# Kernel tuning notes

Hardware: AMD Instinct MI355X
Metric: run time of the kernel (lower is better)

## Reference

```python
import jax, jax.numpy as jnp
import numpy as np

D = 128        # sub_dim
H = D // 2     # attention hidden = max(1, sub_dim // 2)
B = 8192       # molecules per batch
N_ALL = 65536  # unique substructure embeddings
M = 409600     # total selected (mol, substructure) pairs ~ 50 per molecule
T = 12         # num_tasks


def setup_inputs() -> dict:
    key = jax.random.key(0)
    ks = jax.random.split(key, 12)
    s = 0.05
    substructure_feat = jax.random.normal(ks[0], (N_ALL, D), dtype=jnp.float32)
    feat_idx = jax.random.randint(ks[1], (M,), 0, N_ALL)
    batch_idx = jnp.sort(jax.random.randint(ks[2], (M,), 0, B))
    # attention net: Linear(D,H) -> tanh -> Linear(H,1)
    W1 = jax.random.normal(ks[3], (D, H), dtype=jnp.float32) * s
    b1 = jnp.zeros((H,), dtype=jnp.float32)
    W2 = jax.random.normal(ks[4], (H, 1), dtype=jnp.float32) * s
    b2 = jnp.zeros((1,), dtype=jnp.float32)
    # predictor: Linear(D,D) -> (dropout: identity at eval) -> relu -> Linear(D,T)
    W3 = jax.random.normal(ks[5], (D, D), dtype=jnp.float32) * s
    b3 = jnp.zeros((D,), dtype=jnp.float32)
    W4 = jax.random.normal(ks[6], (D, T), dtype=jnp.float32) * s
    b4 = jnp.zeros((T,), dtype=jnp.float32)
    return {
        "substructure_feat": substructure_feat,
        "feat_idx": feat_idx,
        "batch_idx": batch_idx,
        "dim_size": B,
        "W1": W1, "b1": b1, "W2": W2, "b2": b2,
        "W3": W3, "b3": b3, "W4": W4, "b4": b4,
    }


def reference(substructure_feat, feat_idx, batch_idx, dim_size,
              W1, b1, W2, b2, W3, b3, W4, b4):
    # gather selected substructure rows: [M, D]
    x = substructure_feat[feat_idx]
    # attention scores via tiny MLP: [M, 1]
    scores = jnp.tanh(x @ W1 + b1) @ W2 + b2
    # pyg_softmax: per-segment (per-molecule) numerically-stable softmax
    seg_max = jax.ops.segment_max(scores, batch_idx, num_segments=dim_size)  # [B,1]
    e = jnp.exp(scores - seg_max[batch_idx])
    denom = jax.ops.segment_sum(e, batch_idx, num_segments=dim_size)         # [B,1]
    alpha = e / (denom[batch_idx] + 1e-16)                                   # [M,1]
    # scatter-add pooling: [B, D]
    pooled = jax.ops.segment_sum(x * alpha, batch_idx, num_segments=dim_size)
    # predictor (dropout is identity at inference)
    h = jax.nn.relu(pooled @ W3 + b3)
    logits = h @ W4 + b4  # [B, T]
    return logits
```

## Files before the change

kernel.cpp:

```cpp
#include <hip/hip_runtime.h>
#include <hip/hip_bf16.h>
#include <math.h>

#define DD 128
#define HH 64
#define TT 12

typedef __bf16 bf16x8 __attribute__((ext_vector_type(8)));
typedef float  f32x4  __attribute__((ext_vector_type(4)));

__device__ __forceinline__ float fast_tanh(float x) {
    float ex = __expf(2.f * x);
    return (ex - 1.f) * __builtin_amdgcn_rcpf(ex + 1.f);
}

__global__ __launch_bounds__(256) void kMain(
    const int* __restrict__ bidx, int* __restrict__ segs,
    const float* __restrict__ W1, const float* __restrict__ W3,
    __bf16* __restrict__ W3f, const float* __restrict__ W4,
    __bf16* __restrict__ W4f, const float* __restrict__ feat,
    const float* __restrict__ b1, const float* __restrict__ W2,
    const float* __restrict__ b2, float* __restrict__ uexp,
    __bf16* __restrict__ ytab, int M, int B, int N, int nSetup)
{
    __shared__ __bf16 sW1f[16 * 512];
    int tid = threadIdx.x;
    if ((int)blockIdx.x < nSetup) {
        int m = blockIdx.x * 256 + tid;
        if (m < DD * DD) {
            int d = m >> 7, j = m & 127;
            int f = (d >> 5) * 8 + (j >> 4);
            int l = (((d >> 3) & 3) << 4) | (j & 15);
            W3f[f * 512 + l * 8 + (d & 7)] = (__bf16)W3[m];
        }
        if (blockIdx.x == 0) {
            for (int p = tid; p < 4 * 512; p += 256) {
                int f = p >> 9, l = (p >> 3) & 63, e = p & 7;
                int d = 32 * f + 8 * (l >> 4) + e;
                int c = l & 15;
                W4f[p] = (c < TT) ? (__bf16)W4[d * TT + c] : (__bf16)0.f;
            }
            if (tid >= 64 && tid < 128)
                reinterpret_cast<unsigned*>(ytab + (size_t)N * DD)[tid - 64] = 0u;
            if (tid == 0) uexp[N] = 0.f;
        }
        if (m < M) {
            int cur = bidx[m];
            int prev = (m == 0) ? -1 : bidx[m - 1];
            for (int b = prev + 1; b <= cur; ++b) segs[b] = m;
            if (m == M - 1)
                for (int b = cur + 1; b <= B; ++b) segs[b] = M;
        }
        return;
    }
    for (int p = tid; p < HH * DD; p += 256) {
        int d = p >> 6, j = p & 63;
        int f = (d >> 5) * 4 + (j >> 4);
        int l = (((d >> 3) & 3) << 4) | (j & 15);
        sW1f[f * 512 + l * 8 + (d & 7)] = (__bf16)W1[p];
    }
    __syncthreads();
    int sb = blockIdx.x - nSetup;
    int wave = tid >> 6, l = tid & 63;
    int m0 = (sb * 4 + wave) * 16;
    if (m0 >= N) return;
    int r = l & 15, grp = l >> 4;
    int row = min(m0 + r, N - 1);
    const float* xr = feat + (size_t)row * DD + grp * 8;

    bf16x8 a[4];
#pragma unroll
    for (int kk = 0; kk < 4; ++kk) {
        float4 u = *reinterpret_cast<const float4*>(xr + kk * 32);
        float4 v = *reinterpret_cast<const float4*>(xr + kk * 32 + 4);
        bf16x8 t;
        t[0] = (__bf16)u.x; t[1] = (__bf16)u.y; t[2] = (__bf16)u.z; t[3] = (__bf16)u.w;
        t[4] = (__bf16)v.x; t[5] = (__bf16)v.y; t[6] = (__bf16)v.z; t[7] = (__bf16)v.w;
        a[kk] = t;
    }

    f32x4 acc[4] = {};
#pragma unroll
    for (int kk = 0; kk < 4; ++kk) {
#pragma unroll
        for (int g = 0; g < 4; ++g) {
            bf16x8 bfr = *reinterpret_cast<const bf16x8*>(sW1f + (kk * 4 + g) * 512 + l * 8);
            acc[g] = __builtin_amdgcn_mfma_f32_16x16x32_bf16(a[kk], bfr, acc[g], 0, 0, 0);
        }
    }

    float part[4] = {0.f, 0.f, 0.f, 0.f};
#pragma unroll
    for (int g = 0; g < 4; ++g) {
        int j = 16 * g + r;
        float b1j = b1[j], w2j = W2[j];
#pragma unroll
        for (int q = 0; q < 4; ++q)
            part[q] = fmaf(fast_tanh(acc[g][q] + b1j), w2j, part[q]);
    }
#pragma unroll
    for (int q = 0; q < 4; ++q) {
#pragma unroll
        for (int off = 1; off < 16; off <<= 1)
            part[q] += __shfl_xor(part[q], off, 64);
    }
    float v01 = (r & 1) ? part[1] : part[0];
    float v23 = (r & 1) ? part[3] : part[2];
    float vsel = (r & 2) ? v23 : v01;
    float sc = __shfl(vsel, ((r >> 2) << 4) | r, 64);
    float ue = __expf(sc + b2[0]);
    if (grp == 0) uexp[m0 + r] = ue;
    __bf16* dst = ytab + (size_t)row * DD + grp * 8;
#pragma unroll
    for (int kk = 0; kk < 4; ++kk) {
        bf16x8 t;
#pragma unroll
        for (int e = 0; e < 8; ++e) t[e] = (__bf16)(ue * (float)a[kk][e]);
        *reinterpret_cast<bf16x8*>(dst + kk * 32) = t;
    }
}

__global__ __launch_bounds__(512) void kPoolPred(
    const __bf16* __restrict__ ytab, const int* __restrict__ fidx,
    const float* __restrict__ uexp, const int* __restrict__ segs,
    const __bf16* __restrict__ W3f, const __bf16* __restrict__ W4f,
    const float* __restrict__ b3, const float* __restrict__ b4,
    float* __restrict__ out, int B, int NZ, int M)
{
    __shared__ __bf16 psh[16][DD];
    __shared__ __bf16 hsh[16][DD];
    int tid = threadIdx.x;
    int w = tid >> 6, lane = tid & 63;
    int tile = blockIdx.x;
    int sub = lane >> 4, c16 = lane & 15;
    const __bf16* yb = ytab + c16 * 8;

#pragma unroll
    for (int s = 0; s < 2; ++s) {
        int seg = tile * 16 + 2 * w + s;
        int rowit = 2 * w + s;
        float acc[8] = {0.f, 0.f, 0.f, 0.f, 0.f, 0.f, 0.f, 0.f};
        float denl = 0.f;
        if (seg < B) {
            int start = segs[seg], end = segs[seg + 1];
            for (int base = start; base < end; base += 64) {
                int idxs[16];
#pragma unroll
                for (int i = 0; i < 16; ++i) {
                    int p = base + 4 * i + sub;
                    int v = fidx[min(p, M - 1)];
                    idxs[i] = (p < end) ? v : NZ;
                }
                int t = base + lane;
                int fi = (t < end) ? fidx[t] : NZ;
                denl += uexp[fi];
#pragma unroll
                for (int i = 0; i < 16; ++i) {
                    uint4 u4 = *reinterpret_cast<const uint4*>(yb + (size_t)idxs[i] * DD);
                    acc[0] += __builtin_bit_cast(float, u4.x << 16);
                    acc[1] += __builtin_bit_cast(float, u4.x & 0xffff0000u);
                    acc[2] += __builtin_bit_cast(float, u4.y << 16);
                    acc[3] += __builtin_bit_cast(float, u4.y & 0xffff0000u);
                    acc[4] += __builtin_bit_cast(float, u4.z << 16);
                    acc[5] += __builtin_bit_cast(float, u4.z & 0xffff0000u);
                    acc[6] += __builtin_bit_cast(float, u4.w << 16);
                    acc[7] += __builtin_bit_cast(float, u4.w & 0xffff0000u);
                }
            }
        }
        float den = denl;
#pragma unroll
        for (int off = 1; off < 64; off <<= 1) den += __shfl_xor(den, off, 64);
#pragma unroll
        for (int j = 0; j < 8; ++j) {
            acc[j] += __shfl_xor(acc[j], 16, 64);
            acc[j] += __shfl_xor(acc[j], 32, 64);
        }
        if (sub == 0) {
            float inv = 1.f / (den + 1e-16f);
            bf16x8 o;
#pragma unroll
            for (int j = 0; j < 8; ++j) o[j] = (__bf16)(acc[j] * inv);
            *reinterpret_cast<bf16x8*>(&psh[rowit][c16 * 8]) = o;
        }
    }
    __syncthreads();

    if (w != 0) return;
    int r = lane & 15, grp = lane >> 4;
    bf16x8 a[4];
#pragma unroll
    for (int kk = 0; kk < 4; ++kk)
        a[kk] = *reinterpret_cast<const bf16x8*>(&psh[r][kk * 32 + grp * 8]);

    f32x4 acc[8] = {};
#pragma unroll
    for (int kk = 0; kk < 4; ++kk) {
#pragma unroll
        for (int g = 0; g < 8; ++g) {
            bf16x8 bfr = *reinterpret_cast<const bf16x8*>(W3f + (kk * 8 + g) * 512 + lane * 8);
            acc[g] = __builtin_amdgcn_mfma_f32_16x16x32_bf16(a[kk], bfr, acc[g], 0, 0, 0);
        }
    }
#pragma unroll
    for (int g = 0; g < 8; ++g) {
        int j = 16 * g + r;
        float b3j = b3[j];
#pragma unroll
        for (int q = 0; q < 4; ++q)
            hsh[4 * grp + q][j] = (__bf16)fmaxf(acc[g][q] + b3j, 0.f);
    }
    f32x4 acc2 = {};
#pragma unroll
    for (int kk = 0; kk < 4; ++kk) {
        bf16x8 ah = *reinterpret_cast<const bf16x8*>(&hsh[r][kk * 32 + grp * 8]);
        bf16x8 bw = *reinterpret_cast<const bf16x8*>(W4f + kk * 512 + lane * 8);
        acc2 = __builtin_amdgcn_mfma_f32_16x16x32_bf16(ah, bw, acc2, 0, 0, 0);
    }
    int t = r;
    if (t < TT) {
        float b4t = b4[t];
#pragma unroll
        for (int q = 0; q < 4; ++q) {
            int ro = tile * 16 + 4 * grp + q;
            if (ro < B) out[(size_t)ro * TT + t] = acc2[q] + b4t;
        }
    }
}

extern "C" void kernel_launch(void* const* d_in, const int* in_sizes, int n_in,
                              void* d_out, int out_size, void* d_ws, size_t ws_size,
                              hipStream_t stream) {
    const float* feat = (const float*)d_in[0];
    const int*   fidx = (const int*)d_in[1];
    const int*   bidx = (const int*)d_in[2];
    const float* W1 = (const float*)d_in[4];
    const float* b1 = (const float*)d_in[5];
    const float* W2 = (const float*)d_in[6];
    const float* b2 = (const float*)d_in[7];
    const float* W3 = (const float*)d_in[8];
    const float* b3 = (const float*)d_in[9];
    const float* W4 = (const float*)d_in[10];
    const float* b4 = (const float*)d_in[11];

    int N = in_sizes[0] / DD;
    int M = in_sizes[1];
    int B = out_size / TT;
    float* out = (float*)d_out;

    char* ws = (char*)d_ws;
    size_t o = 0;
    auto alloc = [&](size_t bytes) -> char* {
        char* p = ws + o;
        o = (o + bytes + 255) & ~(size_t)255;
        return p;
    };
    float*  uexp = (float*)alloc((size_t)(N + 1) * 4);
    __bf16* W3f  = (__bf16*)alloc(32 * 512 * 2);
    __bf16* W4f  = (__bf16*)alloc(4 * 512 * 2);
    int*    segs = (int*)alloc((size_t)(B + 1) * 4);
    __bf16* ytab = (__bf16*)alloc((size_t)(N + 1) * DD * 2);

    int nSetup = (M + 255) / 256;
    int nScore = (N + 63) / 64;
    kMain<<<nSetup + nScore, 256, 0, stream>>>(bidx, segs, W1, W3, W3f, W4, W4f,
                                               feat, b1, W2, b2, uexp, ytab,
                                               M, B, N, nSetup);
    int ntiles = (B + 15) / 16;
    kPoolPred<<<ntiles, 512, 0, stream>>>(ytab, fidx, uexp, segs, W3f, W4f,
                                          b3, b4, out, B, N, M);
}
```

Before: 39.67 us.

## Process 32 rows per wave in scoring, one segment per wave in pooling

```diff
diff --git a/kernel.cpp b/kernel.cpp
--- a/kernel.cpp
+++ b/kernel.cpp
@@ -21,19 +21,20 @@
     __bf16* __restrict__ W4f, const float* __restrict__ feat,
     const float* __restrict__ b1, const float* __restrict__ W2,
     const float* __restrict__ b2, float* __restrict__ uexp,
-    __bf16* __restrict__ ytab, int M, int B, int N, int nSetup)
+    __bf16* __restrict__ ytab, int M, int B, int N, int nScore)
 {
     __shared__ __bf16 sW1f[16 * 512];
     int tid = threadIdx.x;
-    if ((int)blockIdx.x < nSetup) {
-        int m = blockIdx.x * 256 + tid;
+    if ((int)blockIdx.x >= nScore) {
+        int sb = blockIdx.x - nScore;
+        int m = sb * 256 + tid;
         if (m < DD * DD) {
             int d = m >> 7, j = m & 127;
             int f = (d >> 5) * 8 + (j >> 4);
             int l = (((d >> 3) & 3) << 4) | (j & 15);
             W3f[f * 512 + l * 8 + (d & 7)] = (__bf16)W3[m];
         }
-        if (blockIdx.x == 0) {
+        if (sb == 0) {
             for (int p = tid; p < 4 * 512; p += 256) {
                 int f = p >> 9, l = (p >> 3) & 63, e = p & 7;
                 int d = 32 * f + 8 * (l >> 4) + e;
@@ -60,67 +61,76 @@
         sW1f[f * 512 + l * 8 + (d & 7)] = (__bf16)W1[p];
     }
     __syncthreads();
-    int sb = blockIdx.x - nSetup;
     int wave = tid >> 6, l = tid & 63;
-    int m0 = (sb * 4 + wave) * 16;
+    int m0 = (blockIdx.x * 4 + wave) * 32;
     if (m0 >= N) return;
     int r = l & 15, grp = l >> 4;
-    int row = min(m0 + r, N - 1);
-    const float* xr = feat + (size_t)row * DD + grp * 8;
-
-    bf16x8 a[4];
-#pragma unroll
-    for (int kk = 0; kk < 4; ++kk) {
-        float4 u = *reinterpret_cast<const float4*>(xr + kk * 32);
-        float4 v = *reinterpret_cast<const float4*>(xr + kk * 32 + 4);
-        bf16x8 t;
-        t[0] = (__bf16)u.x; t[1] = (__bf16)u.y; t[2] = (__bf16)u.z; t[3] = (__bf16)u.w;
-        t[4] = (__bf16)v.x; t[5] = (__bf16)v.y; t[6] = (__bf16)v.z; t[7] = (__bf16)v.w;
-        a[kk] = t;
-    }
-
-    f32x4 acc[4] = {};
+
+    bf16x8 a[2][4];
+#pragma unroll
+    for (int hf = 0; hf < 2; ++hf) {
+        int row = min(m0 + hf * 16 + r, N - 1);
+        const float* xr = feat + (size_t)row * DD + grp * 8;
+#pragma unroll
+        for (int kk = 0; kk < 4; ++kk) {
+            float4 u = *reinterpret_cast<const float4*>(xr + kk * 32);
+            float4 v = *reinterpret_cast<const float4*>(xr + kk * 32 + 4);
+            bf16x8 t;
+            t[0] = (__bf16)u.x; t[1] = (__bf16)u.y; t[2] = (__bf16)u.z; t[3] = (__bf16)u.w;
+            t[4] = (__bf16)v.x; t[5] = (__bf16)v.y; t[6] = (__bf16)v.z; t[7] = (__bf16)v.w;
+            a[hf][kk] = t;
+        }
+    }
+
+    f32x4 acc[2][4] = {};
 #pragma unroll
     for (int kk = 0; kk < 4; ++kk) {
 #pragma unroll
         for (int g = 0; g < 4; ++g) {
             bf16x8 bfr = *reinterpret_cast<const bf16x8*>(sW1f + (kk * 4 + g) * 512 + l * 8);
-            acc[g] = __builtin_amdgcn_mfma_f32_16x16x32_bf16(a[kk], bfr, acc[g], 0, 0, 0);
-        }
-    }
-
-    float part[4] = {0.f, 0.f, 0.f, 0.f};
-#pragma unroll
-    for (int g = 0; g < 4; ++g) {
-        int j = 16 * g + r;
-        float b1j = b1[j], w2j = W2[j];
-#pragma unroll
-        for (int q = 0; q < 4; ++q)
-            part[q] = fmaf(fast_tanh(acc[g][q] + b1j), w2j, part[q]);
-    }
-#pragma unroll
-    for (int q = 0; q < 4; ++q) {
-#pragma unroll
-        for (int off = 1; off < 16; off <<= 1)
-            part[q] += __shfl_xor(part[q], off, 64);
-    }
-    float v01 = (r & 1) ? part[1] : part[0];
-    float v23 = (r & 1) ? part[3] : part[2];
-    float vsel = (r & 2) ? v23 : v01;
-    float sc = __shfl(vsel, ((r >> 2) << 4) | r, 64);
-    float ue = __expf(sc + b2[0]);
-    if (grp == 0) uexp[m0 + r] = ue;
-    __bf16* dst = ytab + (size_t)row * DD + grp * 8;
-#pragma unroll
-    for (int kk = 0; kk < 4; ++kk) {
-        bf16x8 t;
-#pragma unroll
-        for (int e = 0; e < 8; ++e) t[e] = (__bf16)(ue * (float)a[kk][e]);
-        *reinterpret_cast<bf16x8*>(dst + kk * 32) = t;
-    }
-}
-
-__global__ __launch_bounds__(512) void kPoolPred(
+            acc[0][g] = __builtin_amdgcn_mfma_f32_16x16x32_bf16(a[0][kk], bfr, acc[0][g], 0, 0, 0);
+            acc[1][g] = __builtin_amdgcn_mfma_f32_16x16x32_bf16(a[1][kk], bfr, acc[1][g], 0, 0, 0);
+        }
+    }
+
+    float b2v = b2[0];
+#pragma unroll
+    for (int hf = 0; hf < 2; ++hf) {
+        float part[4] = {0.f, 0.f, 0.f, 0.f};
+#pragma unroll
+        for (int g = 0; g < 4; ++g) {
+            int j = 16 * g + r;
+            float b1j = b1[j], w2j = W2[j];
+#pragma unroll
+            for (int q = 0; q < 4; ++q)
+                part[q] = fmaf(fast_tanh(acc[hf][g][q] + b1j), w2j, part[q]);
+        }
+#pragma unroll
+        for (int q = 0; q < 4; ++q) {
+#pragma unroll
+            for (int off = 1; off < 16; off <<= 1)
+                part[q] += __shfl_xor(part[q], off, 64);
+        }
+        float v01 = (r & 1) ? part[1] : part[0];
+        float v23 = (r & 1) ? part[3] : part[2];
+        float vsel = (r & 2) ? v23 : v01;
+        float sc = __shfl(vsel, ((r >> 2) << 4) | r, 64);
+        float ue = __expf(sc + b2v);
+        int mh = m0 + hf * 16;
+        if (grp == 0) uexp[mh + r] = ue;
+        int row = min(mh + r, N - 1);
+        __bf16* dst = ytab + (size_t)row * DD + grp * 8;
+#pragma unroll
+        for (int kk = 0; kk < 4; ++kk) {
+            bf16x8 t;
+#pragma unroll
+            for (int e = 0; e < 8; ++e) t[e] = (__bf16)(ue * (float)a[hf][kk][e]);
+            *reinterpret_cast<bf16x8*>(dst + kk * 32) = t;
+        }
+    }
+}
+
+__global__ __launch_bounds__(512, 6) void kPoolPred(
     const __bf16* __restrict__ ytab, const int* __restrict__ fidx,
     const float* __restrict__ uexp, const int* __restrict__ segs,
     const __bf16* __restrict__ W3f, const __bf16* __restrict__ W4f,
@@ -135,54 +145,55 @@
     int sub = lane >> 4, c16 = lane & 15;
     const __bf16* yb = ytab + c16 * 8;
 
-#pragma unroll
-    for (int s = 0; s < 2; ++s) {
-        int seg = tile * 16 + 2 * w + s;
-        int rowit = 2 * w + s;
-        float acc[8] = {0.f, 0.f, 0.f, 0.f, 0.f, 0.f, 0.f, 0.f};
-        float denl = 0.f;
-        if (seg < B) {
-            int start = segs[seg], end = segs[seg + 1];
-            for (int base = start; base < end; base += 64) {
-                int idxs[16];
-#pragma unroll
-                for (int i = 0; i < 16; ++i) {
-                    int p = base + 4 * i + sub;
-                    int v = fidx[min(p, M - 1)];
-                    idxs[i] = (p < end) ? v : NZ;
-                }
-                int t = base + lane;
-                int fi = (t < end) ? fidx[t] : NZ;
-                denl += uexp[fi];
-#pragma unroll
-                for (int i = 0; i < 16; ++i) {
-                    uint4 u4 = *reinterpret_cast<const uint4*>(yb + (size_t)idxs[i] * DD);
-                    acc[0] += __builtin_bit_cast(float, u4.x << 16);
-                    acc[1] += __builtin_bit_cast(float, u4.x & 0xffff0000u);
-                    acc[2] += __builtin_bit_cast(float, u4.y << 16);
-                    acc[3] += __builtin_bit_cast(float, u4.y & 0xffff0000u);
-                    acc[4] += __builtin_bit_cast(float, u4.z << 16);
-                    acc[5] += __builtin_bit_cast(float, u4.z & 0xffff0000u);
-                    acc[6] += __builtin_bit_cast(float, u4.w << 16);
-                    acc[7] += __builtin_bit_cast(float, u4.w & 0xffff0000u);
-                }
+    if (tid < 128) {
+        uint4 z = make_uint4(0u, 0u, 0u, 0u);
+        *reinterpret_cast<uint4*>(&psh[8 + (tid >> 4)][(tid & 15) * 8]) = z;
+    }
+
+    int seg = tile * 8 + w;
+    float acc[8] = {0.f, 0.f, 0.f, 0.f, 0.f, 0.f, 0.f, 0.f};
+    float denl = 0.f;
+    if (seg < B) {
+        int start = segs[seg], end = segs[seg + 1];
+        for (int base = start; base < end; base += 64) {
+            int idxs[16];
+#pragma unroll
+            for (int i = 0; i < 16; ++i) {
+                int p = base + 4 * i + sub;
+                int v = fidx[min(p, M - 1)];
+                idxs[i] = (p < end) ? v : NZ;
             }
-        }
-        float den = denl;
-#pragma unroll
-        for (int off = 1; off < 64; off <<= 1) den += __shfl_xor(den, off, 64);
-#pragma unroll
-        for (int j = 0; j < 8; ++j) {
-            acc[j] += __shfl_xor(acc[j], 16, 64);
-            acc[j] += __shfl_xor(acc[j], 32, 64);
-        }
-        if (sub == 0) {
-            float inv = 1.f / (den + 1e-16f);
-            bf16x8 o;
-#pragma unroll
-            for (int j = 0; j < 8; ++j) o[j] = (__bf16)(acc[j] * inv);
-            *reinterpret_cast<bf16x8*>(&psh[rowit][c16 * 8]) = o;
-        }
+            int t = base + lane;
+            int fi = (t < end) ? fidx[t] : NZ;
+            denl += uexp[fi];
+#pragma unroll
+            for (int i = 0; i < 16; ++i) {
+                uint4 u4 = *reinterpret_cast<const uint4*>(yb + (size_t)idxs[i] * DD);
+                acc[0] += __builtin_bit_cast(float, u4.x << 16);
+                acc[1] += __builtin_bit_cast(float, u4.x & 0xffff0000u);
+                acc[2] += __builtin_bit_cast(float, u4.y << 16);
+                acc[3] += __builtin_bit_cast(float, u4.y & 0xffff0000u);
+                acc[4] += __builtin_bit_cast(float, u4.z << 16);
+                acc[5] += __builtin_bit_cast(float, u4.z & 0xffff0000u);
+                acc[6] += __builtin_bit_cast(float, u4.w << 16);
+                acc[7] += __builtin_bit_cast(float, u4.w & 0xffff0000u);
+            }
+        }
+    }
+    float den = denl;
+#pragma unroll
+    for (int off = 1; off < 64; off <<= 1) den += __shfl_xor(den, off, 64);
+#pragma unroll
+    for (int j = 0; j < 8; ++j) {
+        acc[j] += __shfl_xor(acc[j], 16, 64);
+        acc[j] += __shfl_xor(acc[j], 32, 64);
+    }
+    if (sub == 0) {
+        float inv = 1.f / (den + 1e-16f);
+        bf16x8 o;
+#pragma unroll
+        for (int j = 0; j < 8; ++j) o[j] = (__bf16)(acc[j] * inv);
+        *reinterpret_cast<bf16x8*>(&psh[w][c16 * 8]) = o;
     }
     __syncthreads();
 
@@ -193,13 +204,13 @@
     for (int kk = 0; kk < 4; ++kk)
         a[kk] = *reinterpret_cast<const bf16x8*>(&psh[r][kk * 32 + grp * 8]);
 
-    f32x4 acc[8] = {};
+    f32x4 acc1[8] = {};
 #pragma unroll
     for (int kk = 0; kk < 4; ++kk) {
 #pragma unroll
         for (int g = 0; g < 8; ++g) {
             bf16x8 bfr = *reinterpret_cast<const bf16x8*>(W3f + (kk * 8 + g) * 512 + lane * 8);
-            acc[g] = __builtin_amdgcn_mfma_f32_16x16x32_bf16(a[kk], bfr, acc[g], 0, 0, 0);
+            acc1[g] = __builtin_amdgcn_mfma_f32_16x16x32_bf16(a[kk], bfr, acc1[g], 0, 0, 0);
         }
     }
 #pragma unroll
@@ -208,7 +219,7 @@
         float b3j = b3[j];
 #pragma unroll
         for (int q = 0; q < 4; ++q)
-            hsh[4 * grp + q][j] = (__bf16)fmaxf(acc[g][q] + b3j, 0.f);
+            hsh[4 * grp + q][j] = (__bf16)fmaxf(acc1[g][q] + b3j, 0.f);
     }
     f32x4 acc2 = {};
 #pragma unroll
@@ -217,13 +228,12 @@
         bf16x8 bw = *reinterpret_cast<const bf16x8*>(W4f + kk * 512 + lane * 8);
         acc2 = __builtin_amdgcn_mfma_f32_16x16x32_bf16(ah, bw, acc2, 0, 0, 0);
     }
-    int t = r;
-    if (t < TT) {
-        float b4t = b4[t];
+    if (r < TT && grp < 2) {
+        float b4t = b4[r];
 #pragma unroll
         for (int q = 0; q < 4; ++q) {
-            int ro = tile * 16 + 4 * grp + q;
-            if (ro < B) out[(size_t)ro * TT + t] = acc2[q] + b4t;
+            int ro = tile * 8 + 4 * grp + q;
+            if (ro < B) out[(size_t)ro * TT + r] = acc2[q] + b4t;
         }
     }
 }
@@ -261,12 +271,12 @@
     int*    segs = (int*)alloc((size_t)(B + 1) * 4);
     __bf16* ytab = (__bf16*)alloc((size_t)(N + 1) * DD * 2);
 
+    int nScore = (N + 127) / 128;
     int nSetup = (M + 255) / 256;
-    int nScore = (N + 63) / 64;
-    kMain<<<nSetup + nScore, 256, 0, stream>>>(bidx, segs, W1, W3, W3f, W4, W4f,
+    kMain<<<nScore + nSetup, 256, 0, stream>>>(bidx, segs, W1, W3, W3f, W4, W4f,
                                                feat, b1, W2, b2, uexp, ytab,
-                                               M, B, N, nSetup);
-    int ntiles = (B + 15) / 16;
+                                               M, B, N, nScore);
+    int ntiles = (B + 7) / 8;
     kPoolPred<<<ntiles, 512, 0, stream>>>(ytab, fidx, uexp, segs, W3f, W4f,
                                           b3, b4, out, B, N, M);
 }
```

New measurement: 65.18 us. +64.3%, slower.

## Fuse scoring and pooling kernels into one cooperative launch with grid sync

Applied to the files above, without the earlier changes.

```diff
diff --git a/kernel.cpp b/kernel.cpp
--- a/kernel.cpp
+++ b/kernel.cpp
@@ -1,6 +1,9 @@
 #include <hip/hip_runtime.h>
 #include <hip/hip_bf16.h>
+#include <hip/hip_cooperative_groups.h>
 #include <math.h>
+
+namespace cg = cooperative_groups;
 
 #define DD 128
 #define HH 64
@@ -14,36 +17,32 @@
     return (ex - 1.f) * __builtin_amdgcn_rcpf(ex + 1.f);
 }
 
-__global__ __launch_bounds__(256) void kMain(
+__global__ __launch_bounds__(1024, 4) void kFused(
     const int* __restrict__ bidx, int* __restrict__ segs,
     const float* __restrict__ W1, const float* __restrict__ W3,
     __bf16* __restrict__ W3f, const float* __restrict__ W4,
     __bf16* __restrict__ W4f, const float* __restrict__ feat,
     const float* __restrict__ b1, const float* __restrict__ W2,
     const float* __restrict__ b2, float* __restrict__ uexp,
-    __bf16* __restrict__ ytab, int M, int B, int N, int nSetup)
+    __bf16* __restrict__ ytab, const int* __restrict__ fidx,
+    const float* __restrict__ b3, const float* __restrict__ b4,
+    float* __restrict__ out, int M, int B, int N)
 {
     __shared__ __bf16 sW1f[16 * 512];
     int tid = threadIdx.x;
-    if ((int)blockIdx.x < nSetup) {
-        int m = blockIdx.x * 256 + tid;
-        if (m < DD * DD) {
-            int d = m >> 7, j = m & 127;
-            int f = (d >> 5) * 8 + (j >> 4);
-            int l = (((d >> 3) & 3) << 4) | (j & 15);
-            W3f[f * 512 + l * 8 + (d & 7)] = (__bf16)W3[m];
-        }
-        if (blockIdx.x == 0) {
-            for (int p = tid; p < 4 * 512; p += 256) {
-                int f = p >> 9, l = (p >> 3) & 63, e = p & 7;
-                int d = 32 * f + 8 * (l >> 4) + e;
-                int c = l & 15;
-                W4f[p] = (c < TT) ? (__bf16)W4[d * TT + c] : (__bf16)0.f;
-            }
-            if (tid >= 64 && tid < 128)
-                reinterpret_cast<unsigned*>(ytab + (size_t)N * DD)[tid - 64] = 0u;
-            if (tid == 0) uexp[N] = 0.f;
-        }
+    int bId = blockIdx.x;
+    int wave = tid >> 6, l = tid & 63;
+
+    for (int p = tid; p < HH * DD; p += 1024) {
+        int d = p >> 6, j = p & 63;
+        int f = (d >> 5) * 4 + (j >> 4);
+        int lf = (((d >> 3) & 3) << 4) | (j & 15);
+        sW1f[f * 512 + lf * 8 + (d & 7)] = (__bf16)W1[p];
+    }
+    int gt = bId * 1024 + tid;
+#pragma unroll
+    for (int k = 0; k < 2; ++k) {
+        int m = gt + k * 262144;
         if (m < M) {
             int cur = bidx[m];
             int prev = (m == 0) ? -1 : bidx[m - 1];
@@ -51,94 +50,93 @@
             if (m == M - 1)
                 for (int b = cur + 1; b <= B; ++b) segs[b] = M;
         }
-        return;
-    }
-    for (int p = tid; p < HH * DD; p += 256) {
-        int d = p >> 6, j = p & 63;
-        int f = (d >> 5) * 4 + (j >> 4);
-        int l = (((d >> 3) & 3) << 4) | (j & 15);
-        sW1f[f * 512 + l * 8 + (d & 7)] = (__bf16)W1[p];
+    }
+    if (gt < DD * DD) {
+        int d = gt >> 7, j = gt & 127;
+        int f = (d >> 5) * 8 + (j >> 4);
+        int lf = (((d >> 3) & 3) << 4) | (j & 15);
+        W3f[f * 512 + lf * 8 + (d & 7)] = (__bf16)W3[gt];
+    } else if (gt < DD * DD + 4 * 512) {
+        int p = gt - DD * DD;
+        int f = p >> 9, lf = (p >> 3) & 63, e = p & 7;
+        int d = 32 * f + 8 * (lf >> 4) + e;
+        int c = lf & 15;
+        W4f[p] = (c < TT) ? (__bf16)W4[d * TT + c] : (__bf16)0.f;
+    } else if (gt < DD * DD + 4 * 512 + 16) {
+        reinterpret_cast<uint4*>(ytab + (size_t)N * DD)[gt - (DD * DD + 4 * 512)] =
+            make_uint4(0u, 0u, 0u, 0u);
+    } else if (gt == DD * DD + 4 * 512 + 16) {
+        uexp[N] = 0.f;
     }
     __syncthreads();
-    int sb = blockIdx.x - nSetup;
-    int wave = tid >> 6, l = tid & 63;
-    int m0 = (sb * 4 + wave) * 16;
-    if (m0 >= N) return;
+
+    int m0 = (bId * 16 + wave) * 16;
     int r = l & 15, grp = l >> 4;
-    int row = min(m0 + r, N - 1);
-    const float* xr = feat + (size_t)row * DD + grp * 8;
-
-    bf16x8 a[4];
-#pragma unroll
-    for (int kk = 0; kk < 4; ++kk) {
-        float4 u = *reinterpret_cast<const float4*>(xr + kk * 32);
-        float4 v = *reinterpret_cast<const float4*>(xr + kk * 32 + 4);
-        bf16x8 t;
-        t[0] = (__bf16)u.x; t[1] = (__bf16)u.y; t[2] = (__bf16)u.z; t[3] = (__bf16)u.w;
-        t[4] = (__bf16)v.x; t[5] = (__bf16)v.y; t[6] = (__bf16)v.z; t[7] = (__bf16)v.w;
-        a[kk] = t;
-    }
-
-    f32x4 acc[4] = {};
-#pragma unroll
-    for (int kk = 0; kk < 4; ++kk) {
+    if (m0 < N) {
+        int row = min(m0 + r, N - 1);
+        const float* xr = feat + (size_t)row * DD + grp * 8;
+        bf16x8 a[4];
+#pragma unroll
+        for (int kk = 0; kk < 4; ++kk) {
+            float4 u = *reinterpret_cast<const float4*>(xr + kk * 32);
+            float4 v = *reinterpret_cast<const float4*>(xr + kk * 32 + 4);
+            bf16x8 t;
+            t[0] = (__bf16)u.x; t[1] = (__bf16)u.y; t[2] = (__bf16)u.z; t[3] = (__bf16)u.w;
+            t[4] = (__bf16)v.x; t[5] = (__bf16)v.y; t[6] = (__bf16)v.z; t[7] = (__bf16)v.w;
+            a[kk] = t;
+        }
+        f32x4 acc[4] = {};
+#pragma unroll
+        for (int kk = 0; kk < 4; ++kk) {
+#pragma unroll
+            for (int g = 0; g < 4; ++g) {
+                bf16x8 bfr = *reinterpret_cast<const bf16x8*>(sW1f + (kk * 4 + g) * 512 + l * 8);
+                acc[g] = __builtin_amdgcn_mfma_f32_16x16x32_bf16(a[kk], bfr, acc[g], 0, 0, 0);
+            }
+        }
+        float part[4] = {0.f, 0.f, 0.f, 0.f};
 #pragma unroll
         for (int g = 0; g < 4; ++g) {
-            bf16x8 bfr = *reinterpret_cast<const bf16x8*>(sW1f + (kk * 4 + g) * 512 + l * 8);
-            acc[g] = __builtin_amdgcn_mfma_f32_16x16x32_bf16(a[kk], bfr, acc[g], 0, 0, 0);
-        }
-    }
-
-    float part[4] = {0.f, 0.f, 0.f, 0.f};
-#pragma unroll
-    for (int g = 0; g < 4; ++g) {
-        int j = 16 * g + r;
-        float b1j = b1[j], w2j = W2[j];
-#pragma unroll
-        for (int q = 0; q < 4; ++q)
-            part[q] = fmaf(fast_tanh(acc[g][q] + b1j), w2j, part[q]);
-    }
-#pragma unroll
-    for (int q = 0; q < 4; ++q) {
-#pragma unroll
-        for (int off = 1; off < 16; off <<= 1)
-            part[q] += __shfl_xor(part[q], off, 64);
-    }
-    float v01 = (r & 1) ? part[1] : part[0];
-    float v23 = (r & 1) ? part[3] : part[2];
-    float vsel = (r & 2) ? v23 : v01;
-    float sc = __shfl(vsel, ((r >> 2) << 4) | r, 64);
-    float ue = __expf(sc + b2[0]);
-    if (grp == 0) uexp[m0 + r] = ue;
-    __bf16* dst = ytab + (size_t)row * DD + grp * 8;
-#pragma unroll
-    for (int kk = 0; kk < 4; ++kk) {
-        bf16x8 t;
-#pragma unroll
-        for (int e = 0; e < 8; ++e) t[e] = (__bf16)(ue * (float)a[kk][e]);
-        *reinterpret_cast<bf16x8*>(dst + kk * 32) = t;
-    }
-}
-
-__global__ __launch_bounds__(512) void kPoolPred(
-    const __bf16* __restrict__ ytab, const int* __restrict__ fidx,
-    const float* __restrict__ uexp, const int* __restrict__ segs,
-    const __bf16* __restrict__ W3f, const __bf16* __restrict__ W4f,
-    const float* __restrict__ b3, const float* __restrict__ b4,
-    float* __restrict__ out, int B, int NZ, int M)
-{
-    __shared__ __bf16 psh[16][DD];
-    __shared__ __bf16 hsh[16][DD];
-    int tid = threadIdx.x;
-    int w = tid >> 6, lane = tid & 63;
-    int tile = blockIdx.x;
-    int sub = lane >> 4, c16 = lane & 15;
+            int j = 16 * g + r;
+            float b1j = b1[j], w2j = W2[j];
+#pragma unroll
+            for (int q = 0; q < 4; ++q)
+                part[q] = fmaf(fast_tanh(acc[g][q] + b1j), w2j, part[q]);
+        }
+#pragma unroll
+        for (int q = 0; q < 4; ++q) {
+#pragma unroll
+            for (int off = 1; off < 16; off <<= 1)
+                part[q] += __shfl_xor(part[q], off, 64);
+        }
+        float v01 = (r & 1) ? part[1] : part[0];
+        float v23 = (r & 1) ? part[3] : part[2];
+        float vsel = (r & 2) ? v23 : v01;
+        float sc = __shfl(vsel, ((r >> 2) << 4) | r, 64);
+        float ue = __expf(sc + b2[0]);
+        if (grp == 0) uexp[m0 + r] = ue;
+        __bf16* dst = ytab + (size_t)row * DD + grp * 8;
+#pragma unroll
+        for (int kk = 0; kk < 4; ++kk) {
+            bf16x8 t;
+#pragma unroll
+            for (int e = 0; e < 8; ++e) t[e] = (__bf16)(ue * (float)a[kk][e]);
+            *reinterpret_cast<bf16x8*>(dst + kk * 32) = t;
+        }
+    }
+
+    cg::this_grid().sync();
+
+    typedef __bf16 (*rowArr)[DD];
+    rowArr psh = (rowArr)sW1f;
+    rowArr hsh = (rowArr)(sW1f + 32 * DD);
+    int sub = l >> 4, c16 = l & 15;
     const __bf16* yb = ytab + c16 * 8;
 
 #pragma unroll
     for (int s = 0; s < 2; ++s) {
-        int seg = tile * 16 + 2 * w + s;
-        int rowit = 2 * w + s;
+        int seg = bId * 32 + 2 * wave + s;
+        int rowit = 2 * wave + s;
         float acc[8] = {0.f, 0.f, 0.f, 0.f, 0.f, 0.f, 0.f, 0.f};
         float denl = 0.f;
         if (seg < B) {
@@ -149,10 +147,10 @@
                 for (int i = 0; i < 16; ++i) {
                     int p = base + 4 * i + sub;
                     int v = fidx[min(p, M - 1)];
-                    idxs[i] = (p < end) ? v : NZ;
+                    idxs[i] = (p < end) ? v : N;
                 }
-                int t = base + lane;
-                int fi = (t < end) ? fidx[t] : NZ;
+                int t = base + l;
+                int fi = (t < end) ? fidx[t] : N;
                 denl += uexp[fi];
 #pragma unroll
                 for (int i = 0; i < 16; ++i) {
@@ -186,20 +184,20 @@
     }
     __syncthreads();
 
-    if (w != 0) return;
-    int r = lane & 15, grp = lane >> 4;
-    bf16x8 a[4];
+    if (wave >= 2) return;
+    int rbase = wave * 16;
+    bf16x8 a2[4];
 #pragma unroll
     for (int kk = 0; kk < 4; ++kk)
-        a[kk] = *reinterpret_cast<const bf16x8*>(&psh[r][kk * 32 + grp * 8]);
-
-    f32x4 acc[8] = {};
+        a2[kk] = *reinterpret_cast<const bf16x8*>(&psh[rbase + r][kk * 32 + grp * 8]);
+
+    f32x4 acc1[8] = {};
 #pragma unroll
     for (int kk = 0; kk < 4; ++kk) {
 #pragma unroll
         for (int g = 0; g < 8; ++g) {
-            bf16x8 bfr = *reinterpret_cast<const bf16x8*>(W3f + (kk * 8 + g) * 512 + lane * 8);
-            acc[g] = __builtin_amdgcn_mfma_f32_16x16x32_bf16(a[kk], bfr, acc[g], 0, 0, 0);
+            bf16x8 bfr = *reinterpret_cast<const bf16x8*>(W3f + (kk * 8 + g) * 512 + l * 8);
+            acc1[g] = __builtin_amdgcn_mfma_f32_16x16x32_bf16(a2[kk], bfr, acc1[g], 0, 0, 0);
         }
     }
 #pragma unroll
@@ -208,22 +206,21 @@
         float b3j = b3[j];
 #pragma unroll
         for (int q = 0; q < 4; ++q)
-            hsh[4 * grp + q][j] = (__bf16)fmaxf(acc[g][q] + b3j, 0.f);
+            hsh[rbase + 4 * grp + q][j] = (__bf16)fmaxf(acc1[g][q] + b3j, 0.f);
     }
     f32x4 acc2 = {};
 #pragma unroll
     for (int kk = 0; kk < 4; ++kk) {
-        bf16x8 ah = *reinterpret_cast<const bf16x8*>(&hsh[r][kk * 32 + grp * 8]);
-        bf16x8 bw = *reinterpret_cast<const bf16x8*>(W4f + kk * 512 + lane * 8);
+        bf16x8 ah = *reinterpret_cast<const bf16x8*>(&hsh[rbase + r][kk * 32 + grp * 8]);
+        bf16x8 bw = *reinterpret_cast<const bf16x8*>(W4f + kk * 512 + l * 8);
         acc2 = __builtin_amdgcn_mfma_f32_16x16x32_bf16(ah, bw, acc2, 0, 0, 0);
     }
-    int t = r;
-    if (t < TT) {
-        float b4t = b4[t];
+    if (r < TT) {
+        float b4t = b4[r];
 #pragma unroll
         for (int q = 0; q < 4; ++q) {
-            int ro = tile * 16 + 4 * grp + q;
-            if (ro < B) out[(size_t)ro * TT + t] = acc2[q] + b4t;
+            int ro = bId * 32 + rbase + 4 * grp + q;
+            if (ro < B) out[(size_t)ro * TT + r] = acc2[q] + b4t;
         }
     }
 }
@@ -231,8 +228,6 @@
 extern "C" void kernel_launch(void* const* d_in, const int* in_sizes, int n_in,
                               void* d_out, int out_size, void* d_ws, size_t ws_size,
                               hipStream_t stream) {
-    const float* feat = (const float*)d_in[0];
-    const int*   fidx = (const int*)d_in[1];
     const int*   bidx = (const int*)d_in[2];
     const float* W1 = (const float*)d_in[4];
     const float* b1 = (const float*)d_in[5];
@@ -242,6 +237,8 @@
     const float* b3 = (const float*)d_in[9];
     const float* W4 = (const float*)d_in[10];
     const float* b4 = (const float*)d_in[11];
+    const float* feat = (const float*)d_in[0];
+    const int*   fidx = (const int*)d_in[1];
 
     int N = in_sizes[0] / DD;
     int M = in_sizes[1];
@@ -261,12 +258,12 @@
     int*    segs = (int*)alloc((size_t)(B + 1) * 4);
     __bf16* ytab = (__bf16*)alloc((size_t)(N + 1) * DD * 2);
 
-    int nSetup = (M + 255) / 256;
-    int nScore = (N + 63) / 64;
-    kMain<<<nSetup + nScore, 256, 0, stream>>>(bidx, segs, W1, W3, W3f, W4, W4f,
-                                               feat, b1, W2, b2, uexp, ytab,
-                                               M, B, N, nSetup);
-    int ntiles = (B + 15) / 16;
-    kPoolPred<<<ntiles, 512, 0, stream>>>(ytab, fidx, uexp, segs, W3f, W4f,
-                                          b3, b4, out, B, N, M);
+    void* args[] = {
+        (void*)&bidx, (void*)&segs, (void*)&W1, (void*)&W3, (void*)&W3f,
+        (void*)&W4, (void*)&W4f, (void*)&feat, (void*)&b1, (void*)&W2,
+        (void*)&b2, (void*)&uexp, (void*)&ytab, (void*)&fidx,
+        (void*)&b3, (void*)&b4, (void*)&out, (void*)&M, (void*)&B, (void*)&N
+    };
+    hipLaunchCooperativeKernel((const void*)kFused, dim3(256), dim3(1024),
+                               args, 0, stream);
 }
```

Measured after the change: 82.03 us. 107% more time.
